# Performance work log

Measured on AMD Instinct MI355X. Metric: run time of the kernel, lower is better.

The kernel has to match this reference:

```python
import jax, jax.numpy as jnp
import numpy as np

N, F, R, H, C = 16384, 128, 16, 8, 64
E = 163840
SELF_LOOP_FILL = 0.5
NEG_SLOPE = 0.2


def _glorot(key, shape):
    fan = shape[0] + shape[-1]
    lim = jnp.sqrt(6.0 / fan)
    return jax.random.uniform(key, shape, jnp.float32, -lim, lim)


def setup_inputs() -> dict:
    key = jax.random.key(0)
    ks = jax.random.split(key, 20)
    inp = {
        'x': jax.random.normal(ks[0], (N, F), jnp.float32),
        'edge_index': jax.random.randint(ks[1], (2, E), 0, N, jnp.int64),
        'edge_attr': jax.random.uniform(ks[2], (E, R), jnp.float32),
        # layer 1 (concat=True): in=F, out per head=C, heads=H
        'Wl1': _glorot(ks[3], (F, H * C)), 'bl1': jnp.zeros((H * C,), jnp.float32),
        'Wr1': _glorot(ks[4], (F, H * C)), 'br1': jnp.zeros((H * C,), jnp.float32),
        'We1': _glorot(ks[5], (R, H * C)),
        'att1': _glorot(ks[6], (H, C)),
        'bias1': jnp.zeros((H * C,), jnp.float32),
        # layer 2 (concat=False): in=H*C
        'Wl2': _glorot(ks[7], (H * C, H * C)), 'bl2': jnp.zeros((H * C,), jnp.float32),
        'Wr2': _glorot(ks[8], (H * C, H * C)), 'br2': jnp.zeros((H * C,), jnp.float32),
        'We2': _glorot(ks[9], (R, H * C)),
        'att2': _glorot(ks[10], (H, C)),
        'bias2': jnp.zeros((C,), jnp.float32),
    }
    return inp


def gatv2_layer(x, src, dst, e, Wl, bl, Wr, br, We, att, bias, concat):
    n = x.shape[0]
    h, c = att.shape
    xl = (x @ Wl + bl).reshape(n, h, c)   # source transform (used for messages)
    xr = (x @ Wr + br).reshape(n, h, c)   # target transform
    ep = (e @ We).reshape(-1, h, c)       # edge feature transform [E',H,C]
    z = jax.nn.leaky_relu(xl[src] + xr[dst] + ep, NEG_SLOPE)  # [E',H,C]
    logits = jnp.einsum('ehc,hc->eh', z, att)                 # [E',H]
    # softmax over incoming edges of each destination node
    m = jax.ops.segment_max(logits, dst, num_segments=n)
    m = jax.lax.stop_gradient(jnp.where(jnp.isfinite(m), m, 0.0))
    ex = jnp.exp(logits - m[dst])
    denom = jax.ops.segment_sum(ex, dst, num_segments=n)
    alpha = ex / (denom[dst] + 1e-16)                         # [E',H]
    out = jax.ops.segment_sum(xl[src] * alpha[..., None], dst, num_segments=n)  # [N,H,C]
    out = out.reshape(n, h * c) if concat else out.mean(axis=1)
    return out + bias


def reference(x, edge_index, edge_attr, Wl1, bl1, Wr1, br1, We1, att1, bias1,
              Wl2, bl2, Wr2, br2, We2, att2, bias2):
    n = x.shape[0]
    loops = jnp.arange(n, dtype=edge_index.dtype)
    src = jnp.concatenate([edge_index[0], loops])
    dst = jnp.concatenate([edge_index[1], loops])
    e = jnp.concatenate([edge_attr, jnp.full((n, edge_attr.shape[1]), SELF_LOOP_FILL, edge_attr.dtype)])
    out = gatv2_layer(x, src, dst, e, Wl1, bl1, Wr1, br1, We1, att1, bias1, concat=True)
    out = gatv2_layer(out, src, dst, e, Wl2, bl2, Wr2, br2, We2, att2, bias2, concat=False)
    return out
```

## Files before the change

### kernel.cpp

```cpp
#include <hip/hip_runtime.h>
#include <cstdint>

#define NN 16384
#define FF 128
#define RR 16
#define HH 8
#define CC 64
#define HC 512
#define NC 1024
#define EE 163840
#define ET (EE + NN)

typedef __attribute__((ext_vector_type(2))) float f32x2;
typedef __attribute__((ext_vector_type(4))) float f32x4;
typedef __attribute__((ext_vector_type(8))) short short8;

__device__ __forceinline__ unsigned short f2bf(float f) {
  unsigned u = __builtin_bit_cast(unsigned, f);
  u = (u + 0x7FFFu + ((u >> 16) & 1u)) >> 16;
  return (unsigned short)u;
}
__device__ __forceinline__ float bf2f(unsigned short b) {
  unsigned u = ((unsigned)b) << 16;
  return __builtin_bit_cast(float, u);
}

__device__ __forceinline__ void gl_lds16(const void* g, void* l) {
  __builtin_amdgcn_global_load_lds(
      (const __attribute__((address_space(1))) unsigned int*)g,
      (__attribute__((address_space(3))) unsigned int*)l, 16, 0, 0);
}

__global__ __launch_bounds__(256) void count_kernel(const int* __restrict__ ei,
                                                    int* __restrict__ counts) {
  int e = blockIdx.x * 256 + threadIdx.x;
  if (e >= ET) return;
  int d = (e < EE) ? ei[EE + e] : (e - EE);
  atomicAdd(&counts[d], 1);
}

__global__ __launch_bounds__(1024) void scan_kernel(const int* __restrict__ counts,
                                                    int* __restrict__ offs,
                                                    int* __restrict__ cursor) {
  __shared__ int part[1024];
  int t = threadIdx.x;
  int base = t * 16;
  int loc[16];
  int s = 0;
#pragma unroll
  for (int i = 0; i < 16; ++i) { loc[i] = s; s += counts[base + i]; }
  part[t] = s;
  __syncthreads();
  for (int off = 1; off < 1024; off <<= 1) {
    int v = (t >= off) ? part[t - off] : 0;
    __syncthreads();
    part[t] += v;
    __syncthreads();
  }
  int excl = part[t] - s;
#pragma unroll
  for (int i = 0; i < 16; ++i) {
    int o = excl + loc[i];
    offs[base + i] = o;
    cursor[base + i] = o;
  }
  if (t == 1023) offs[NN] = part[1023];
}

__global__ __launch_bounds__(256) void scatter_kernel(const int* __restrict__ ei,
                                                      int* __restrict__ cursor,
                                                      int* __restrict__ csr,
                                                      int* __restrict__ srcc) {
  int e = blockIdx.x * 256 + threadIdx.x;
  if (e >= ET) return;
  int s, d;
  if (e < EE) { s = ei[e]; d = ei[EE + e]; }
  else        { s = d = e - EE; }
  int p = atomicAdd(&cursor[d], 1);
  csr[p] = e;
  srcc[p] = s;
}

__global__ __launch_bounds__(256) void pack_a_kernel(const float* __restrict__ A,
                                                     unsigned short* __restrict__ Ah,
                                                     unsigned short* __restrict__ Al,
                                                     int K) {
  int nkb = K >> 5;
  int rb = blockIdx.x / nkb, kb = blockIdx.x % nkb;
  int t = threadIdx.x;
  size_t obase = ((size_t)rb * nkb + kb) * 4096;
#pragma unroll
  for (int u = 0; u < 2; ++u) {
    int lin = t + u * 256;
    int r = lin >> 2, ch = lin & 3;
    int chs = (ch + (r >> 1)) & 3;
    const float* src = &A[(size_t)(rb * 128 + r) * K + kb * 32 + ch * 8];
    float4 v0 = *(const float4*)src;
    float4 v1 = *(const float4*)(src + 4);
    float v[8] = {v0.x, v0.y, v0.z, v0.w, v1.x, v1.y, v1.z, v1.w};
    short8 hv, lv;
#pragma unroll
    for (int j = 0; j < 8; ++j) {
      unsigned short h = f2bf(v[j]);
      unsigned short l = f2bf(v[j] - bf2f(h));
      hv[j] = (short)h; lv[j] = (short)l;
    }
    size_t o = obase + (size_t)r * 32 + chs * 8;
    *(short8*)&Ah[o] = hv;
    *(short8*)&Al[o] = lv;
  }
}

__global__ __launch_bounds__(256) void pack_w_kernel(const float* __restrict__ Wl,
                                                     const float* __restrict__ Wr,
                                                     unsigned short* __restrict__ Bh,
                                                     unsigned short* __restrict__ Bl,
                                                     int K) {
  int nkb = K >> 5;
  int nb = blockIdx.x / nkb, kb = blockIdx.x % nkb;
  int t = threadIdx.x;
  size_t obase = ((size_t)nb * nkb + kb) * 4096;
#pragma unroll
  for (int u = 0; u < 2; ++u) {
    int lin = t + u * 256;
    int n = lin >> 2, ch = lin & 3;
    int chs = (ch + (n >> 1)) & 3;
    int gn = nb * 128 + n;
    const float* W = (gn < HC) ? Wl : Wr;
    int cn = gn & (HC - 1);
    short8 hv, lv;
#pragma unroll
    for (int j = 0; j < 8; ++j) {
      float f = W[(size_t)(kb * 32 + ch * 8 + j) * HC + cn];
      unsigned short h = f2bf(f);
      unsigned short l = f2bf(f - bf2f(h));
      hv[j] = (short)h; lv[j] = (short)l;
    }
    size_t o = obase + (size_t)n * 32 + chs * 8;
    *(short8*)&Bh[o] = hv;
    *(short8*)&Bl[o] = lv;
  }
}

__global__ __launch_bounds__(256) void pack_wet_kernel(const float* __restrict__ We,
                                                       float* __restrict__ WeT) {
  int i = blockIdx.x * 256 + threadIdx.x;
  int c = i >> 4, r = i & 15;
  WeT[i] = We[r * HC + c];
}

__global__ __launch_bounds__(256) void gemm_mfma_kernel(const unsigned short* __restrict__ Ah,
                                                        const unsigned short* __restrict__ Al,
                                                        const unsigned short* __restrict__ Bh,
                                                        const unsigned short* __restrict__ Bl,
                                                        const float* __restrict__ bl,
                                                        const float* __restrict__ br,
                                                        float* __restrict__ C, int K) {
  __shared__ unsigned short lAh[4096], lAl[4096], lBh[4096], lBl[4096];
  int tid = threadIdx.x;
  int wave = tid >> 6, lane = tid & 63;
  int l15 = lane & 15, quad = lane >> 4;
  int wm = wave >> 1, wn = wave & 1;
  int nb = blockIdx.x, rb = blockIdx.y;
  int nkb = K >> 5;

  const unsigned short* src = (wave == 0) ? Ah : (wave == 1) ? Al : (wave == 2) ? Bh : Bl;
  unsigned short* dst = (wave == 0) ? lAh : (wave == 1) ? lAl : (wave == 2) ? lBh : lBl;
  int blk = (wave < 2) ? rb : nb;
  size_t gstep = 4096;
  const unsigned short* gbase = src + ((size_t)blk * nkb) * gstep + lane * 8;

  f32x4 acc[4][4];
#pragma unroll
  for (int i = 0; i < 4; ++i)
#pragma unroll
    for (int j = 0; j < 4; ++j) acc[i][j] = (f32x4){0.f, 0.f, 0.f, 0.f};

  int offA[4], offB[4];
#pragma unroll
  for (int t = 0; t < 4; ++t) {
    int ra = wm * 64 + t * 16 + l15;
    offA[t] = ra * 32 + ((quad + (ra >> 1)) & 3) * 8;
    int rbn = wn * 64 + t * 16 + l15;
    offB[t] = rbn * 32 + ((quad + (rbn >> 1)) & 3) * 8;
  }

  for (int kb = 0; kb < nkb; ++kb) {
    const unsigned short* g = gbase + (size_t)kb * gstep;
#pragma unroll
    for (int i = 0; i < 8; ++i)
      gl_lds16(g + i * 512, dst + i * 512);
    __syncthreads();

    short8 ah[4], al_[4], bh[4], bl_[4];
#pragma unroll
    for (int t = 0; t < 4; ++t) {
      ah[t]  = *(const short8*)&lAh[offA[t]];
      al_[t] = *(const short8*)&lAl[offA[t]];
      bh[t]  = *(const short8*)&lBh[offB[t]];
      bl_[t] = *(const short8*)&lBl[offB[t]];
    }
#pragma unroll
    for (int tm = 0; tm < 4; ++tm)
#pragma unroll
      for (int tn = 0; tn < 4; ++tn) {
        acc[tm][tn] = __builtin_amdgcn_mfma_f32_16x16x32_bf16(ah[tm], bh[tn], acc[tm][tn], 0, 0, 0);
        acc[tm][tn] = __builtin_amdgcn_mfma_f32_16x16x32_bf16(ah[tm], bl_[tn], acc[tm][tn], 0, 0, 0);
        acc[tm][tn] = __builtin_amdgcn_mfma_f32_16x16x32_bf16(al_[tm], bh[tn], acc[tm][tn], 0, 0, 0);
      }
    __syncthreads();
  }

#pragma unroll
  for (int tm = 0; tm < 4; ++tm) {
    int row = rb * 128 + wm * 64 + tm * 16 + quad * 4;
#pragma unroll
    for (int tn = 0; tn < 4; ++tn) {
      int col = nb * 128 + wn * 64 + tn * 16 + l15;
      float bias = (col < HC) ? bl[col] : br[col - HC];
#pragma unroll
      for (int r = 0; r < 4; ++r)
        C[(size_t)(row + r) * NC + col] = acc[tm][tn][r] + bias;
    }
  }
}


__device__ __forceinline__ void fused_edge_body(
    const int* __restrict__ csr, const int* __restrict__ srcc,
    const int* __restrict__ offs, const float* __restrict__ eattr,
    const float* __restrict__ WeT, const float* __restrict__ att,
    const float* __restrict__ xlr, int n, int t,
    float& out0, float& out1) {
  int c0 = t * 2;
  int beg = offs[n], end = offs[n + 1];
  f32x2 wf0[8], wf1[8];
  {
    const f32x2* w0 = (const f32x2*)&WeT[(size_t)c0 * RR];
    const f32x2* w1 = (const f32x2*)&WeT[(size_t)(c0 + 1) * RR];
#pragma unroll
    for (int j = 0; j < 8; ++j) { wf0[j] = w0[j]; wf1[j] = w1[j]; }
  }
  float2 amv = *(const float2*)&att[c0];
  f32x2 rv = *(const f32x2*)&xlr[(size_t)n * NC + HC + c0];
  float m = -1e30f, l = 0.f;
  f32x2 acc = (f32x2){0.f, 0.f};
#pragma unroll 2
  for (int i = beg; i < end; ++i) {
    int e = csr[i];
    int s = srcc[i];
    f32x2 lv = *(const f32x2*)&xlr[(size_t)s * NC + c0];
    f32x2 e2[8];
    if (e < EE) {
      const f32x2* ep2 = (const f32x2*)&eattr[(size_t)e * RR];
#pragma unroll
      for (int j = 0; j < 8; ++j) e2[j] = ep2[j];
    } else {
#pragma unroll
      for (int j = 0; j < 8; ++j) e2[j] = (f32x2){0.5f, 0.5f};
    }
    f32x2 epp0 = (f32x2){0.f, 0.f};
    f32x2 epp1 = (f32x2){0.f, 0.f};
#pragma unroll
    for (int j = 0; j < 8; ++j) {
      epp0 = __builtin_elementwise_fma(e2[j], wf0[j], epp0);
      epp1 = __builtin_elementwise_fma(e2[j], wf1[j], epp1);
    }
    f32x2 base2 = lv + rv;
    float z0 = base2.x + (epp0.x + epp0.y);
    float z1 = base2.y + (epp1.x + epp1.y);
    z0 = fmaf(0.2f, fminf(z0, 0.f), fmaxf(z0, 0.f));
    z1 = fmaf(0.2f, fminf(z1, 0.f), fmaxf(z1, 0.f));
    float p = fmaf(z0, amv.x, z1 * amv.y);
    p += __shfl_xor(p, 1);
    p += __shfl_xor(p, 2);
    p += __shfl_xor(p, 4);
    p += __shfl_xor(p, 8);
    p += __shfl_xor(p, 16);
    float nm = fmaxf(m, p);
    float sc = __expf(m - nm);
    float el = __expf(p - nm);
    l = l * sc + el;
    acc.x = acc.x * sc + el * lv.x;
    acc.y = acc.y * sc + el * lv.y;
    m = nm;
  }
  float inv = 1.f / (l + 1e-16f);
  out0 = acc.x * inv;
  out1 = acc.y * inv;
}

__global__ __launch_bounds__(256) void fused_concat_kernel(
    const int* __restrict__ csr, const int* __restrict__ srcc,
    const int* __restrict__ offs, const float* __restrict__ eattr,
    const float* __restrict__ WeT, const float* __restrict__ att,
    const float* __restrict__ xlr, const float* __restrict__ bias,
    unsigned short* __restrict__ Ah2, unsigned short* __restrict__ Al2) {
  int n = blockIdx.x, t = threadIdx.x;
  float o0, o1;
  fused_edge_body(csr, srcc, offs, eattr, WeT, att, xlr, n, t, o0, o1);
  int c0 = t * 2;
  float v0 = o0 + bias[c0];
  float v1 = o1 + bias[c0 + 1];
  int r = n & 127, rbk = n >> 7;
#pragma unroll
  for (int u = 0; u < 2; ++u) {
    int c = c0 + u;
    float v = u ? v1 : v0;
    int kb = c >> 5, ch = (c >> 3) & 3, j = c & 7;
    int chs = (ch + (r >> 1)) & 3;
    size_t idx = ((size_t)rbk * 16 + kb) * 4096 + (size_t)r * 32 + chs * 8 + j;
    unsigned short h = f2bf(v);
    Ah2[idx] = h;
    Al2[idx] = f2bf(v - bf2f(h));
  }
}

__global__ __launch_bounds__(256) void fused_mean_kernel(
    const int* __restrict__ csr, const int* __restrict__ srcc,
    const int* __restrict__ offs, const float* __restrict__ eattr,
    const float* __restrict__ WeT, const float* __restrict__ att,
    const float* __restrict__ xlr, const float* __restrict__ bias2,
    float* __restrict__ out) {
  __shared__ float red[HC];
  int n = blockIdx.x, t = threadIdx.x;
  float o0, o1;
  fused_edge_body(csr, srcc, offs, eattr, WeT, att, xlr, n, t, o0, o1);
  int c0 = t * 2;
  red[c0] = o0;
  red[c0 + 1] = o1;
  __syncthreads();
  if (t < CC) {
    float ssum = 0.f;
#pragma unroll
    for (int hh = 0; hh < HH; ++hh) ssum += red[hh * CC + t];
    out[(size_t)n * CC + t] = ssum * 0.125f + bias2[t];
  }
}

extern "C" void kernel_launch(void* const* d_in, const int* in_sizes, int n_in,
                              void* d_out, int out_size, void* d_ws, size_t ws_size,
                              hipStream_t stream) {
  const float* x     = (const float*)d_in[0];
  const int*   ei    = (const int*)d_in[1];
  const float* eattr = (const float*)d_in[2];
  const float* Wl1   = (const float*)d_in[3];
  const float* bl1   = (const float*)d_in[4];
  const float* Wr1   = (const float*)d_in[5];
  const float* br1   = (const float*)d_in[6];
  const float* We1   = (const float*)d_in[7];
  const float* att1  = (const float*)d_in[8];
  const float* bias1 = (const float*)d_in[9];
  const float* Wl2   = (const float*)d_in[10];
  const float* bl2   = (const float*)d_in[11];
  const float* Wr2   = (const float*)d_in[12];
  const float* br2   = (const float*)d_in[13];
  const float* We2   = (const float*)d_in[14];
  const float* att2  = (const float*)d_in[15];
  const float* bias2 = (const float*)d_in[16];
  float* out = (float*)d_out;

  char* ws = (char*)d_ws;
  size_t off = 0;
  auto alloc = [&](size_t bytes) {
    char* p = ws + off;
    off += (bytes + 255) & ~(size_t)255;
    return p;
  };
  float* bufC = (float*)alloc((size_t)NN * NC * 4);
  unsigned short* Ah1 = (unsigned short*)alloc((size_t)NN * FF * 2);
  unsigned short* Al1 = (unsigned short*)alloc((size_t)NN * FF * 2);
  unsigned short* Ah2 = (unsigned short*)alloc((size_t)NN * HC * 2);
  unsigned short* Al2 = (unsigned short*)alloc((size_t)NN * HC * 2);
  unsigned short* Wh1 = (unsigned short*)alloc((size_t)FF * NC * 2);
  unsigned short* Wlo1 = (unsigned short*)alloc((size_t)FF * NC * 2);
  unsigned short* Wh2 = (unsigned short*)alloc((size_t)HC * NC * 2);
  unsigned short* Wlo2 = (unsigned short*)alloc((size_t)HC * NC * 2);
  float* WeT1 = (float*)alloc((size_t)HC * RR * 4);
  float* WeT2 = (float*)alloc((size_t)HC * RR * 4);
  int* counts = (int*)alloc((size_t)NN * 4);
  int* offs   = (int*)alloc((size_t)(NN + 1) * 4);
  int* cursor = (int*)alloc((size_t)NN * 4);
  int* csr    = (int*)alloc((size_t)ET * 4);
  int* srcc   = (int*)alloc((size_t)ET * 4);
  (void)ws_size; (void)in_sizes; (void)n_in; (void)out_size;

  hipMemsetAsync(counts, 0, (size_t)NN * 4, stream);
  int eb = (ET + 255) / 256;
  count_kernel<<<eb, 256, 0, stream>>>(ei, counts);
  scan_kernel<<<1, 1024, 0, stream>>>(counts, offs, cursor);
  scatter_kernel<<<eb, 256, 0, stream>>>(ei, cursor, csr, srcc);

  pack_a_kernel<<<(NN / 128) * (FF / 32), 256, 0, stream>>>(x, Ah1, Al1, FF);
  pack_w_kernel<<<(NC / 128) * (FF / 32), 256, 0, stream>>>(Wl1, Wr1, Wh1, Wlo1, FF);
  pack_w_kernel<<<(NC / 128) * (HC / 32), 256, 0, stream>>>(Wl2, Wr2, Wh2, Wlo2, HC);
  pack_wet_kernel<<<(HC * RR) / 256, 256, 0, stream>>>(We1, WeT1);
  pack_wet_kernel<<<(HC * RR) / 256, 256, 0, stream>>>(We2, WeT2);

  dim3 ggrid(NC / 128, NN / 128);

  gemm_mfma_kernel<<<ggrid, 256, 0, stream>>>(Ah1, Al1, Wh1, Wlo1, bl1, br1, bufC, FF);
  fused_concat_kernel<<<NN, 256, 0, stream>>>(csr, srcc, offs, eattr, WeT1, att1, bufC, bias1, Ah2, Al2);

  gemm_mfma_kernel<<<ggrid, 256, 0, stream>>>(Ah2, Al2, Wh2, Wlo2, bl2, br2, bufC, HC);
  fused_mean_kernel<<<NN, 256, 0, stream>>>(csr, srcc, offs, eattr, WeT2, att2, bufC, bias2, out);
}
```

Before: 462.4 us.

## Stage edge attributes and sources in LDS per 64-edge chunk, process edges pairwise

The per-node edge loop now loads up to 64 edges' attribute rows and source indices cooperatively into shared memory, instead of every thread redundantly reading the full 16-float edge row from global memory. Edges are then processed two at a time with a merged online-softmax update, which exposes more independent loads and exp work. Waves-per-EU is pinned to 4 to steer register allocation. This adds block-level syncs per chunk and shared-memory use, and the pinned occupancy may constrain the compiler.

```diff
diff --git a/kernel.cpp b/kernel.cpp
--- a/kernel.cpp
+++ b/kernel.cpp
@@ -226,12 +226,44 @@
 }
 
 
+__device__ __forceinline__ float edge_logit(const float* ser,
+                                            const f32x2* wf0, const f32x2* wf1,
+                                            float2 amv, f32x2 lv, f32x2 rv) {
+  const f32x4* e4 = (const f32x4*)ser;
+  f32x4 a = e4[0], b = e4[1], c = e4[2], d = e4[3];
+  f32x2 er[8];
+  er[0] = (f32x2){a.x, a.y}; er[1] = (f32x2){a.z, a.w};
+  er[2] = (f32x2){b.x, b.y}; er[3] = (f32x2){b.z, b.w};
+  er[4] = (f32x2){c.x, c.y}; er[5] = (f32x2){c.z, c.w};
+  er[6] = (f32x2){d.x, d.y}; er[7] = (f32x2){d.z, d.w};
+  f32x2 q0 = (f32x2){0.f, 0.f};
+  f32x2 q1 = (f32x2){0.f, 0.f};
+#pragma unroll
+  for (int j = 0; j < 8; ++j) {
+    q0 = __builtin_elementwise_fma(er[j], wf0[j], q0);
+    q1 = __builtin_elementwise_fma(er[j], wf1[j], q1);
+  }
+  float z0 = lv.x + rv.x + (q0.x + q0.y);
+  float z1 = lv.y + rv.y + (q1.x + q1.y);
+  z0 = fmaf(0.2f, fminf(z0, 0.f), fmaxf(z0, 0.f));
+  z1 = fmaf(0.2f, fminf(z1, 0.f), fmaxf(z1, 0.f));
+  float p = fmaf(z0, amv.x, z1 * amv.y);
+  p += __shfl_xor(p, 1);
+  p += __shfl_xor(p, 2);
+  p += __shfl_xor(p, 4);
+  p += __shfl_xor(p, 8);
+  p += __shfl_xor(p, 16);
+  return p;
+}
+
 __device__ __forceinline__ void fused_edge_body(
     const int* __restrict__ csr, const int* __restrict__ srcc,
     const int* __restrict__ offs, const float* __restrict__ eattr,
     const float* __restrict__ WeT, const float* __restrict__ att,
     const float* __restrict__ xlr, int n, int t,
     float& out0, float& out1) {
+  __shared__ float se[64][16];
+  __shared__ int ssrc[64];
   int c0 = t * 2;
   int beg = offs[n], end = offs[n + 1];
   f32x2 wf0[8], wf1[8];
@@ -245,52 +277,57 @@
   f32x2 rv = *(const f32x2*)&xlr[(size_t)n * NC + HC + c0];
   float m = -1e30f, l = 0.f;
   f32x2 acc = (f32x2){0.f, 0.f};
-#pragma unroll 2
-  for (int i = beg; i < end; ++i) {
-    int e = csr[i];
-    int s = srcc[i];
-    f32x2 lv = *(const f32x2*)&xlr[(size_t)s * NC + c0];
-    f32x2 e2[8];
-    if (e < EE) {
-      const f32x2* ep2 = (const f32x2*)&eattr[(size_t)e * RR];
-#pragma unroll
-      for (int j = 0; j < 8; ++j) e2[j] = ep2[j];
-    } else {
-#pragma unroll
-      for (int j = 0; j < 8; ++j) e2[j] = (f32x2){0.5f, 0.5f};
-    }
-    f32x2 epp0 = (f32x2){0.f, 0.f};
-    f32x2 epp1 = (f32x2){0.f, 0.f};
-#pragma unroll
-    for (int j = 0; j < 8; ++j) {
-      epp0 = __builtin_elementwise_fma(e2[j], wf0[j], epp0);
-      epp1 = __builtin_elementwise_fma(e2[j], wf1[j], epp1);
-    }
-    f32x2 base2 = lv + rv;
-    float z0 = base2.x + (epp0.x + epp0.y);
-    float z1 = base2.y + (epp1.x + epp1.y);
-    z0 = fmaf(0.2f, fminf(z0, 0.f), fmaxf(z0, 0.f));
-    z1 = fmaf(0.2f, fminf(z1, 0.f), fmaxf(z1, 0.f));
-    float p = fmaf(z0, amv.x, z1 * amv.y);
-    p += __shfl_xor(p, 1);
-    p += __shfl_xor(p, 2);
-    p += __shfl_xor(p, 4);
-    p += __shfl_xor(p, 8);
-    p += __shfl_xor(p, 16);
-    float nm = fmaxf(m, p);
-    float sc = __expf(m - nm);
-    float el = __expf(p - nm);
-    l = l * sc + el;
-    acc.x = acc.x * sc + el * lv.x;
-    acc.y = acc.y * sc + el * lv.y;
-    m = nm;
+  for (int cb = beg; cb < end; cb += 64) {
+    int cnt = end - cb;
+    if (cnt > 64) cnt = 64;
+    if (cb > beg) __syncthreads();
+    if (t < cnt) ssrc[t] = srcc[cb + t];
+    for (int q = t; q < cnt * 4; q += 256) {
+      int i = q >> 2, r4 = (q & 3) << 2;
+      int e = csr[cb + i];
+      float4 v;
+      if (e < EE) v = *(const float4*)&eattr[(size_t)e * RR + r4];
+      else        v = make_float4(0.5f, 0.5f, 0.5f, 0.5f);
+      *(float4*)&se[i][r4] = v;
+    }
+    __syncthreads();
+    int i = 0;
+    for (; i + 2 <= cnt; i += 2) {
+      int s0 = ssrc[i], s1 = ssrc[i + 1];
+      f32x2 lv0 = *(const f32x2*)&xlr[(size_t)s0 * NC + c0];
+      f32x2 lv1 = *(const f32x2*)&xlr[(size_t)s1 * NC + c0];
+      float p0 = edge_logit(se[i],     wf0, wf1, amv, lv0, rv);
+      float p1 = edge_logit(se[i + 1], wf0, wf1, amv, lv1, rv);
+      float nm = fmaxf(fmaxf(m, p0), p1);
+      float sc = __expf(m - nm);
+      float e0 = __expf(p0 - nm);
+      float e1 = __expf(p1 - nm);
+      l = l * sc + e0 + e1;
+      acc.x = acc.x * sc + e0 * lv0.x + e1 * lv1.x;
+      acc.y = acc.y * sc + e0 * lv0.y + e1 * lv1.y;
+      m = nm;
+    }
+    if (i < cnt) {
+      int s0 = ssrc[i];
+      f32x2 lv0 = *(const f32x2*)&xlr[(size_t)s0 * NC + c0];
+      float p0 = edge_logit(se[i], wf0, wf1, amv, lv0, rv);
+      float nm = fmaxf(m, p0);
+      float sc = __expf(m - nm);
+      float e0 = __expf(p0 - nm);
+      l = l * sc + e0;
+      acc.x = acc.x * sc + e0 * lv0.x;
+      acc.y = acc.y * sc + e0 * lv0.y;
+      m = nm;
+    }
   }
   float inv = 1.f / (l + 1e-16f);
   out0 = acc.x * inv;
   out1 = acc.y * inv;
 }
 
-__global__ __launch_bounds__(256) void fused_concat_kernel(
+__global__ __launch_bounds__(256)
+__attribute__((amdgpu_waves_per_eu(4, 4)))
+void fused_concat_kernel(
     const int* __restrict__ csr, const int* __restrict__ srcc,
     const int* __restrict__ offs, const float* __restrict__ eattr,
     const float* __restrict__ WeT, const float* __restrict__ att,
@@ -316,7 +353,9 @@
   }
 }
 
-__global__ __launch_bounds__(256) void fused_mean_kernel(
+__global__ __launch_bounds__(256)
+__attribute__((amdgpu_waves_per_eu(4, 4)))
+void fused_mean_kernel(
     const int* __restrict__ csr, const int* __restrict__ srcc,
     const int* __restrict__ offs, const float* __restrict__ eattr,
     const float* __restrict__ WeT, const float* __restrict__ att,
```

After: 494.4 us. 1.07x slower.
